# Kernel tuning notes

Hardware: AMD Instinct MI355X
Metric: run time of the kernel (lower is better)

## Reference

```python
import jax, jax.numpy as jnp
import numpy as np

B, S, D = 4, 2048, 1024
H = 16
HD = D // H          # 64
HALF = HD // 2       # 32


def _rope(t, cos, sin):
    # t: [B, S, H, HD]; cos/sin: [S, HALF]
    tr = t.reshape(*t.shape[:-1], HALF, 2)
    t0, t1 = tr[..., 0], tr[..., 1]
    c = cos[None, :, None, :]
    s = sin[None, :, None, :]
    out = jnp.stack([t0 * c - t1 * s, t0 * s + t1 * c], axis=-1)
    return out.reshape(t.shape)


def setup_inputs() -> dict:
    key = jax.random.key(0)
    ks = jax.random.split(key, 7)
    x = jax.random.normal(ks[0], (B, S, D), dtype=jnp.float32)
    # rotary tables (theta=10000 convention)
    inv_freq = 1.0 / (10000.0 ** (np.arange(0, HD, 2, dtype=np.float32) / HD))
    angles = np.arange(S, dtype=np.float32)[:, None] * inv_freq[None, :]
    freqs_cos = jnp.asarray(np.cos(angles))
    freqs_sin = jnp.asarray(np.sin(angles))
    scale = 1.0 / np.sqrt(D)
    wq = jax.random.normal(ks[1], (D, D), dtype=jnp.float32) * scale
    wk = jax.random.normal(ks[2], (D, D), dtype=jnp.float32) * scale
    wv = jax.random.normal(ks[3], (D, D), dtype=jnp.float32) * scale
    wo = jax.random.normal(ks[4], (D, D), dtype=jnp.float32) * scale
    return {"x": x, "freqs_cos": freqs_cos, "freqs_sin": freqs_sin,
            "wq": wq, "wk": wk, "wv": wv, "wo": wo}


def reference(x, freqs_cos, freqs_sin, wq, wk, wv, wo):
    b, s, d = x.shape
    q = (x @ wq.T).reshape(b, s, H, HD)
    k = (x @ wk.T).reshape(b, s, H, HD)
    v = (x @ wv.T).reshape(b, s, H, HD)
    q = _rope(q, freqs_cos, freqs_sin)
    k = _rope(k, freqs_cos, freqs_sin)
    # [B, H, S, HD]
    q = q.transpose(0, 2, 1, 3)
    k = k.transpose(0, 2, 1, 3)
    v = v.transpose(0, 2, 1, 3)
    scores = jnp.einsum("bhqd,bhkd->bhqk", q, k) / jnp.sqrt(jnp.float32(HD))
    causal = jnp.tril(jnp.ones((s, s), dtype=bool))
    scores = jnp.where(causal[None, None, :, :], scores, jnp.finfo(scores.dtype).min)
    attn = jax.nn.softmax(scores, axis=-1)
    out = jnp.einsum("bhqk,bhkd->bhqd", attn, v)
    out = out.transpose(0, 2, 1, 3).reshape(b, s, d)
    return out @ wo.T
```

## Files before the change

kernel.cpp:

```cpp
#include <hip/hip_runtime.h>
#include <hip/hip_bf16.h>
#include <cstdint>
#include <cstddef>

#define BB 4
#define SS 2048
#define DD 1024
#define HH 16
#define HDD 64

typedef __bf16 bf16_t;
typedef __bf16 bf16x8 __attribute__((ext_vector_type(8)));
typedef float f32x4 __attribute__((ext_vector_type(4)));
typedef unsigned u32x2 __attribute__((ext_vector_type(2)));

__device__ __forceinline__ unsigned short f2bf(float f) {
    unsigned u = __float_as_uint(f);
    unsigned r = (u + 0x7FFFu + ((u >> 16) & 1u)) >> 16;
    return (unsigned short)r;
}
__device__ __forceinline__ bf16_t f2bf16(float f) {
    return __builtin_bit_cast(bf16_t, f2bf(f));
}
__device__ __forceinline__ bf16x8 cvt8(float4 a, float4 b) {
    bf16x8 r;
    r[0] = f2bf16(a.x); r[1] = f2bf16(a.y);
    r[2] = f2bf16(a.z); r[3] = f2bf16(a.w);
    r[4] = f2bf16(b.x); r[5] = f2bf16(b.y);
    r[6] = f2bf16(b.z); r[7] = f2bf16(b.w);
    return r;
}
__device__ __forceinline__ unsigned cvtpk_bf16(float lo, float hi) {
    unsigned r;
    asm("v_cvt_pk_bf16_f32 %0, %1, %2" : "=v"(r) : "v"(lo), "v"(hi));
    return r;
}
__device__ __forceinline__ float exp2_raw(float x) {
    float r;
    asm("v_exp_f32 %0, %1" : "=v"(r) : "v"(x));
    return r;
}

#define GLL16(gp, lp)                                                          \
    __builtin_amdgcn_global_load_lds(                                          \
        (const __attribute__((address_space(1))) void*)(gp),                   \
        (__attribute__((address_space(3))) void*)(lp), 16, 0, 0)

__global__ __launch_bounds__(256) void cvt1(const float* __restrict__ in,
                                            bf16_t* __restrict__ out) {
    size_t i = (size_t)blockIdx.x * 256 + threadIdx.x;
    const float4* p = (const float4*)in + i * 2;
    *(bf16x8*)(out + i * 8) = cvt8(p[0], p[1]);
}
__global__ __launch_bounds__(256) void cvt4(
    const float* __restrict__ w0, const float* __restrict__ w1,
    const float* __restrict__ w2, const float* __restrict__ w3,
    bf16_t* __restrict__ o0, bf16_t* __restrict__ o1,
    bf16_t* __restrict__ o2, bf16_t* __restrict__ o3) {
    const float* in = blockIdx.y == 0 ? w0 : blockIdx.y == 1 ? w1
                    : blockIdx.y == 2 ? w2 : w3;
    bf16_t* out = blockIdx.y == 0 ? o0 : blockIdx.y == 1 ? o1
                : blockIdx.y == 2 ? o2 : o3;
    size_t i = (size_t)blockIdx.x * 256 + threadIdx.x;
    const float4* p = (const float4*)in + i * 2;
    *(bf16x8*)(out + i * 8) = cvt8(p[0], p[1]);
}

__global__ __launch_bounds__(256, 2) void gemm_qkv(
    const bf16_t* __restrict__ A, const bf16_t* __restrict__ Wall,
    bf16_t* __restrict__ Qb, bf16_t* __restrict__ Kb,
    bf16_t* __restrict__ Vt,
    const float* __restrict__ fcos, const float* __restrict__ fsin,
    float qscale)
{
    constexpr int K = 1024;
    __shared__ alignas(16) bf16_t lA[128 * 64];
    __shared__ alignas(16) bf16_t lB[128 * 64];

    const int tid  = threadIdx.x;
    const int w    = tid >> 6;
    const int lane = tid & 63;
    const int quad = lane >> 4;
    const int l16  = lane & 15;
    const int wm   = w >> 1;
    const int wn   = w & 1;
    const int m0   = blockIdx.y * 128;
    const int n0   = blockIdx.x * 128;
    const int sub  = n0 >> 10;

    f32x4 acc[4][4];
#pragma unroll
    for (int i = 0; i < 4; i++)
#pragma unroll
        for (int j = 0; j < 4; j++) acc[i][j] = (f32x4){0.f, 0.f, 0.f, 0.f};

    const int srow8 = lane >> 3;
    const int slot  = lane & 7;

    for (int k0 = 0; k0 < K; k0 += 64) {
#pragma unroll
        for (int i = 0; i < 4; ++i) {
            int row = w * 32 + i * 8;
            GLL16(A + (size_t)(m0 + row + srow8) * K + k0 + slot * 8,
                  &lA[row * 64]);
            GLL16(Wall + (size_t)(n0 + row + srow8) * K + k0 + slot * 8,
                  &lB[row * 64]);
        }
        __syncthreads();
#pragma unroll
        for (int kk = 0; kk < 2; ++kk) {
            bf16x8 af[4], bfr[4];
#pragma unroll
            for (int mt = 0; mt < 4; ++mt)
                af[mt] = *(const bf16x8*)
                    &lA[(wm * 64 + mt * 16 + l16) * 64 + (kk * 4 + quad) * 8];
#pragma unroll
            for (int nt = 0; nt < 4; ++nt)
                bfr[nt] = *(const bf16x8*)
                    &lB[(wn * 64 + nt * 16 + l16) * 64 + (kk * 4 + quad) * 8];
#pragma unroll
            for (int mt = 0; mt < 4; ++mt)
#pragma unroll
                for (int nt = 0; nt < 4; ++nt)
                    acc[mt][nt] = __builtin_amdgcn_mfma_f32_16x16x32_bf16(
                        af[mt], bfr[nt], acc[mt][nt], 0, 0, 0);
        }
        __syncthreads();
    }

    if (sub < 2) {
        unsigned short* Cu = (unsigned short*)(sub == 0 ? Qb : Kb);
        const float scale = sub == 0 ? qscale : 1.0f;
#pragma unroll
        for (int mt = 0; mt < 4; ++mt) {
#pragma unroll
            for (int nt = 0; nt < 4; ++nt) {
                int col  = (n0 & 1023) + wn * 64 + nt * 16 + l16;
                int h    = col >> 6;
                int d    = col & 63;
                int pidx = d >> 1;
                bool even = (col & 1) == 0;
#pragma unroll
                for (int r = 0; r < 4; ++r) {
                    int m = m0 + wm * 64 + mt * 16 + quad * 4 + r;
                    int b = m >> 11;
                    int s = m & 2047;
                    float v  = acc[mt][nt][r];
                    float p  = __shfl_xor(v, 1);
                    float c  = fcos[s * 32 + pidx];
                    float sn = fsin[s * 32 + pidx];
                    float o  = even ? (v * c - p * sn) : (p * sn + v * c);
                    Cu[(size_t)((b * HH + h) * SS + s) * HDD + d] =
                        f2bf(o * scale);
                }
            }
        }
    } else {
        unsigned short* Cu = (unsigned short*)Vt;
#pragma unroll
        for (int mt = 0; mt < 4; ++mt) {
#pragma unroll
            for (int nt = 0; nt < 4; ++nt) {
                int col = (n0 & 1023) + wn * 64 + nt * 16 + l16;
                int h = col >> 6, d = col & 63;
#pragma unroll
                for (int r = 0; r < 4; ++r) {
                    int m = m0 + wm * 64 + mt * 16 + quad * 4 + r;
                    int b = m >> 11, s = m & 2047;
                    Cu[(size_t)((b * HH + h) * HDD + d) * SS + s] =
                        f2bf(acc[mt][nt][r]);
                }
            }
        }
    }
}

__global__ __launch_bounds__(256, 2) void gemm_out(
    const bf16_t* __restrict__ A, const bf16_t* __restrict__ W,
    float* __restrict__ Cf)
{
    constexpr int K = 1024, N = 1024;
    __shared__ alignas(16) bf16_t lA[128 * 64];
    __shared__ alignas(16) bf16_t lB[128 * 64];

    const int tid  = threadIdx.x;
    const int w    = tid >> 6;
    const int lane = tid & 63;
    const int quad = lane >> 4;
    const int l16  = lane & 15;
    const int wm   = w >> 1;
    const int wn   = w & 1;
    const int m0   = blockIdx.y * 128;
    const int n0   = blockIdx.x * 128;

    f32x4 acc[4][4];
#pragma unroll
    for (int i = 0; i < 4; i++)
#pragma unroll
        for (int j = 0; j < 4; j++) acc[i][j] = (f32x4){0.f, 0.f, 0.f, 0.f};

    const int srow8 = lane >> 3;
    const int slot  = lane & 7;

    for (int k0 = 0; k0 < K; k0 += 64) {
#pragma unroll
        for (int i = 0; i < 4; ++i) {
            int row = w * 32 + i * 8;
            GLL16(A + (size_t)(m0 + row + srow8) * K + k0 + slot * 8,
                  &lA[row * 64]);
            GLL16(W + (size_t)(n0 + row + srow8) * K + k0 + slot * 8,
                  &lB[row * 64]);
        }
        __syncthreads();
#pragma unroll
        for (int kk = 0; kk < 2; ++kk) {
            bf16x8 af[4], bfr[4];
#pragma unroll
            for (int mt = 0; mt < 4; ++mt)
                af[mt] = *(const bf16x8*)
                    &lA[(wm * 64 + mt * 16 + l16) * 64 + (kk * 4 + quad) * 8];
#pragma unroll
            for (int nt = 0; nt < 4; ++nt)
                bfr[nt] = *(const bf16x8*)
                    &lB[(wn * 64 + nt * 16 + l16) * 64 + (kk * 4 + quad) * 8];
#pragma unroll
            for (int mt = 0; mt < 4; ++mt)
#pragma unroll
                for (int nt = 0; nt < 4; ++nt)
                    acc[mt][nt] = __builtin_amdgcn_mfma_f32_16x16x32_bf16(
                        af[mt], bfr[nt], acc[mt][nt], 0, 0, 0);
        }
        __syncthreads();
    }

#pragma unroll
    for (int mt = 0; mt < 4; ++mt) {
        int mrow = m0 + wm * 64 + mt * 16 + quad * 4;
#pragma unroll
        for (int nt = 0; nt < 4; ++nt) {
            int col = n0 + wn * 64 + nt * 16 + l16;
#pragma unroll
            for (int r = 0; r < 4; ++r)
                Cf[(size_t)(mrow + r) * N + col] = acc[mt][nt][r];
        }
    }
}

__global__ __launch_bounds__(256, 2) void attn(
    const bf16_t* __restrict__ Q, const bf16_t* __restrict__ Kt,
    const bf16_t* __restrict__ Vt, bf16_t* __restrict__ O)
{
    __shared__ alignas(16) bf16_t lK[128 * 64];
    __shared__ alignas(16) bf16_t lV[2][64 * 64];

    const int tid  = threadIdx.x;
    const int w    = tid >> 6;
    const int lane = tid & 63;
    const int quad = lane >> 4;
    const int l16  = lane & 15;

    const int blk  = blockIdx.x;
    const int xcd  = blk & 7;
    const int rest = blk >> 3;
    const int g    = rest & 7;
    const int bh   = ((rest >> 3) << 3) | xcd;

    const int b = bh >> 4, h = bh & 15;
    unsigned short* Ou = (unsigned short*)O;
    const bf16_t* Qb = Q  + (size_t)bh * SS * HDD;
    const bf16_t* Kb = Kt + (size_t)bh * SS * HDD;
    const bf16_t* Vb = Vt + (size_t)bh * HDD * SS;

    const int row8 = lane >> 3;
    const int chk  = lane & 7;

    for (int phase = 0; phase < 2; ++phase) {
        const int Tp  = phase ? 15 - g : g;
        const int q0  = Tp * 128 + w * 32;
        const int nkb = Tp + 1;

        bf16x8 qf[2][2];
#pragma unroll
        for (int qs = 0; qs < 2; ++qs) {
            const bf16_t* qp =
                Qb + (size_t)(q0 + qs * 16 + l16) * HDD + quad * 8;
            qf[qs][0] = *(const bf16x8*)(qp);
            qf[qs][1] = *(const bf16x8*)(qp + 32);
        }

        f32x4 o[2][4];
        float ps[2];
#pragma unroll
        for (int qs = 0; qs < 2; ++qs) {
            ps[qs] = 0.f;
#pragma unroll
            for (int i = 0; i < 4; ++i) o[qs][i] = (f32x4){0.f, 0.f, 0.f, 0.f};
        }

        for (int t = 0; t < nkb; ++t) {
            const int kb2 = t * 128;

#pragma unroll
            for (int i = 0; i < 4; ++i) {
                int rbase = w * 32 + i * 8;
                int row   = rbase + row8;
                GLL16(Kb + (size_t)(kb2 + row) * HDD + ((chk ^ (row & 7)) * 8),
                      &lK[rbase * 64]);
            }
#pragma unroll
            for (int pp = 0; pp < 2; ++pp)
#pragma unroll
                for (int i = 0; i < 2; ++i) {
                    int rbase = w * 16 + i * 8;
                    int row   = rbase + row8;
                    GLL16(Vb + (size_t)row * SS + kb2 + pp * 64 +
                              ((chk ^ (row & 7)) * 8),
                          &lV[pp][rbase * 64]);
                }
            __syncthreads();

#pragma unroll
            for (int p = 0; p < 2; ++p) {
                const int kbp = kb2 + p * 64;
                if (kbp < q0 + 32) {
                    const bool diag = (kbp + 63 > q0);

                    bf16x8 kf[4][2];
#pragma unroll
                    for (int nt = 0; nt < 4; ++nt) {
                        const int row = p * 64 + nt * 16 + l16;
#pragma unroll
                        for (int hf = 0; hf < 2; ++hf)
                            kf[nt][hf] = *(const bf16x8*)
                                &lK[row * 64 +
                                    (((hf * 4 + quad) ^ (row & 7)) * 8)];
                    }

                    unsigned pk[4][2][2];
#pragma unroll
                    for (int nt = 0; nt < 4; ++nt) {
                        const int krow = kbp + nt * 16 + quad * 4;
#pragma unroll
                        for (int qs = 0; qs < 2; ++qs) {
                            f32x4 s = (f32x4){0.f, 0.f, 0.f, 0.f};
                            s = __builtin_amdgcn_mfma_f32_16x16x32_bf16(
                                kf[nt][0], qf[qs][0], s, 0, 0, 0);
                            s = __builtin_amdgcn_mfma_f32_16x16x32_bf16(
                                kf[nt][1], qf[qs][1], s, 0, 0, 0);
                            if (diag) {
                                const int qcol = q0 + qs * 16 + l16;
#pragma unroll
                                for (int r = 0; r < 4; ++r)
                                    if (krow + r > qcol) s[r] = -1e30f;
                            }
                            float ev[4];
#pragma unroll
                            for (int r = 0; r < 4; ++r) {
                                float e = exp2_raw(s[r]);
                                ps[qs] += e;
                                ev[r] = e;
                            }
                            pk[nt][qs][0] = cvtpk_bf16(ev[0], ev[1]);
                            pk[nt][qs][1] = cvtpk_bf16(ev[2], ev[3]);
                        }
                    }

#pragma unroll
                    for (int kk = 0; kk < 2; ++kk) {
                        bf16x8 vfk[4];
#pragma unroll
                        for (int nt = 0; nt < 4; ++nt) {
                            const int row = nt * 16 + l16;
                            vfk[nt] = *(const bf16x8*)
                                &lV[p][row * 64 +
                                       (((kk * 4 + quad) ^ (row & 7)) * 8)];
                        }
#pragma unroll
                        for (int qs = 0; qs < 2; ++qs) {
                            u32x2 sA = __builtin_amdgcn_permlane32_swap(
                                pk[2 * kk][qs][0], pk[2 * kk + 1][qs][0],
                                false, false);
                            u32x2 sB = __builtin_amdgcn_permlane32_swap(
                                pk[2 * kk][qs][1], pk[2 * kk + 1][qs][1],
                                false, false);
                            u32x2 tA = __builtin_amdgcn_permlane16_swap(
                                sA.x, sA.y, false, false);
                            u32x2 tB = __builtin_amdgcn_permlane16_swap(
                                sB.x, sB.y, false, false);
                            union { unsigned d[4]; bf16x8 v; } pf;
                            pf.d[0] = tA.x;
                            pf.d[1] = tB.x;
                            pf.d[2] = tA.y;
                            pf.d[3] = tB.y;
#pragma unroll
                            for (int nt = 0; nt < 4; ++nt)
                                o[qs][nt] =
                                    __builtin_amdgcn_mfma_f32_16x16x32_bf16(
                                        pf.v, vfk[nt], o[qs][nt], 0, 0, 0);
                        }
                    }
                }
            }
            __syncthreads();
        }

#pragma unroll
        for (int qs = 0; qs < 2; ++qs) {
            float tsum = ps[qs];
            tsum += __shfl_xor(tsum, 16);
            tsum += __shfl_xor(tsum, 32);
            float inv[4];
#pragma unroll
            for (int r = 0; r < 4; ++r)
                inv[r] = 1.0f / __shfl(tsum, quad * 4 + r);
#pragma unroll
            for (int nt = 0; nt < 4; ++nt) {
                int d = nt * 16 + l16;
#pragma unroll
                for (int r = 0; r < 4; ++r) {
                    int s = q0 + qs * 16 + quad * 4 + r;
                    Ou[(size_t)(b * SS + s) * DD + h * HDD + d] =
                        f2bf(o[qs][nt][r] * inv[r]);
                }
            }
        }
    }
}

extern "C" void kernel_launch(void* const* d_in, const int* in_sizes, int n_in,
                              void* d_out, int out_size, void* d_ws,
                              size_t ws_size, hipStream_t stream)
{
    const float* x    = (const float*)d_in[0];
    const float* fcos = (const float*)d_in[1];
    const float* fsin = (const float*)d_in[2];
    const float* wq   = (const float*)d_in[3];
    const float* wk   = (const float*)d_in[4];
    const float* wv   = (const float*)d_in[5];
    const float* wo   = (const float*)d_in[6];

    char* ws = (char*)d_ws;
    const size_t TSZ = (size_t)BB * SS * DD * sizeof(bf16_t);
    const size_t WSZ = (size_t)DD * DD * sizeof(bf16_t);
    bf16_t* Qb  = (bf16_t*)(ws);
    bf16_t* Kb  = (bf16_t*)(ws + TSZ);
    bf16_t* Ob  = (bf16_t*)(ws + 2 * TSZ);
    bf16_t* wb0 = (bf16_t*)(ws + 3 * TSZ);
    bf16_t* wb1 = (bf16_t*)(ws + 3 * TSZ + WSZ);
    bf16_t* wb2 = (bf16_t*)(ws + 3 * TSZ + 2 * WSZ);
    bf16_t* wb3 = (bf16_t*)(ws + 3 * TSZ + 3 * WSZ);
    bf16_t* xb  = (bf16_t*)d_out;
    bf16_t* Vt  = (bf16_t*)((char*)d_out + TSZ);

    dim3 bb(256);
    cvt1<<<dim3(4096), bb, 0, stream>>>(x, xb);
    cvt4<<<dim3(512, 4), bb, 0, stream>>>(wq, wk, wv, wo, wb0, wb1, wb2, wb3);

    const float sscale = 0.125f * 1.44269504088896f;
    gemm_qkv<<<dim3(24, 64), bb, 0, stream>>>(xb, wb0, Qb, Kb, Vt,
                                              fcos, fsin, sscale);
    attn<<<dim3(512), bb, 0, stream>>>(Qb, Kb, Vt, Ob);
    gemm_out<<<dim3(8, 64), bb, 0, stream>>>(Ob, wb3, (float*)d_out);
}
```

Measured before the change: 251.0 us.

## XOR-swizzle GEMM LDS tiles, remap block order per XCD, merge conversion kernels

Applies an XOR swizzle to the 16-byte chunk index when staging A and B tiles into LDS and when reading them back, so MFMA fragment reads spread across banks instead of conflicting. Remaps the linear block index in both GEMMs so consecutive blocks dispatched to the same XCD cover nearby tiles, which should improve L2 reuse. Merges the input and weight fp32-to-bf16 conversion kernels into one launch. The remap assumes round-robin dispatch across eight XCDs and grid sizes divisible by eight.

```diff
diff --git a/kernel.cpp b/kernel.cpp
--- a/kernel.cpp
+++ b/kernel.cpp
@@ -46,22 +46,28 @@
         (const __attribute__((address_space(1))) void*)(gp),                   \
         (__attribute__((address_space(3))) void*)(lp), 16, 0, 0)
 
-__global__ __launch_bounds__(256) void cvt1(const float* __restrict__ in,
-                                            bf16_t* __restrict__ out) {
-    size_t i = (size_t)blockIdx.x * 256 + threadIdx.x;
-    const float4* p = (const float4*)in + i * 2;
-    *(bf16x8*)(out + i * 8) = cvt8(p[0], p[1]);
-}
-__global__ __launch_bounds__(256) void cvt4(
+__global__ __launch_bounds__(256) void cvtall(
+    const float* __restrict__ x,
     const float* __restrict__ w0, const float* __restrict__ w1,
     const float* __restrict__ w2, const float* __restrict__ w3,
+    bf16_t* __restrict__ xb,
     bf16_t* __restrict__ o0, bf16_t* __restrict__ o1,
-    bf16_t* __restrict__ o2, bf16_t* __restrict__ o3) {
-    const float* in = blockIdx.y == 0 ? w0 : blockIdx.y == 1 ? w1
-                    : blockIdx.y == 2 ? w2 : w3;
-    bf16_t* out = blockIdx.y == 0 ? o0 : blockIdx.y == 1 ? o1
-                : blockIdx.y == 2 ? o2 : o3;
-    size_t i = (size_t)blockIdx.x * 256 + threadIdx.x;
+    bf16_t* __restrict__ o2, bf16_t* __restrict__ o3)
+{
+    const int bx = blockIdx.x;
+    const float* in;
+    bf16_t* out;
+    size_t i;
+    if (bx < 4096) {
+        in = x; out = xb;
+        i = (size_t)bx * 256 + threadIdx.x;
+    } else {
+        const int g = bx - 4096;
+        const int s = g >> 9;
+        in  = s == 0 ? w0 : s == 1 ? w1 : s == 2 ? w2 : w3;
+        out = s == 0 ? o0 : s == 1 ? o1 : s == 2 ? o2 : o3;
+        i = (size_t)(g & 511) * 256 + threadIdx.x;
+    }
     const float4* p = (const float4*)in + i * 2;
     *(bf16x8*)(out + i * 8) = cvt8(p[0], p[1]);
 }
@@ -84,9 +90,12 @@
     const int l16  = lane & 15;
     const int wm   = w >> 1;
     const int wn   = w & 1;
-    const int m0   = blockIdx.y * 128;
-    const int n0   = blockIdx.x * 128;
-    const int sub  = n0 >> 10;
+
+    const int lid     = blockIdx.y * 24 + blockIdx.x;
+    const int logical = (lid & 7) * 192 + (lid >> 3);
+    const int m0      = (logical / 24) * 128;
+    const int n0      = (logical % 24) * 128;
+    const int sub     = n0 >> 10;
 
     f32x4 acc[4][4];
 #pragma unroll
@@ -100,24 +109,28 @@
     for (int k0 = 0; k0 < K; k0 += 64) {
 #pragma unroll
         for (int i = 0; i < 4; ++i) {
-            int row = w * 32 + i * 8;
-            GLL16(A + (size_t)(m0 + row + srow8) * K + k0 + slot * 8,
-                  &lA[row * 64]);
-            GLL16(Wall + (size_t)(n0 + row + srow8) * K + k0 + slot * 8,
-                  &lB[row * 64]);
+            int rbase = w * 32 + i * 8;
+            int row   = rbase + srow8;
+            int sc    = (slot ^ (row & 7)) * 8;
+            GLL16(A + (size_t)(m0 + row) * K + k0 + sc, &lA[rbase * 64]);
+            GLL16(Wall + (size_t)(n0 + row) * K + k0 + sc, &lB[rbase * 64]);
         }
         __syncthreads();
 #pragma unroll
         for (int kk = 0; kk < 2; ++kk) {
             bf16x8 af[4], bfr[4];
 #pragma unroll
-            for (int mt = 0; mt < 4; ++mt)
+            for (int mt = 0; mt < 4; ++mt) {
+                const int row = wm * 64 + mt * 16 + l16;
                 af[mt] = *(const bf16x8*)
-                    &lA[(wm * 64 + mt * 16 + l16) * 64 + (kk * 4 + quad) * 8];
-#pragma unroll
-            for (int nt = 0; nt < 4; ++nt)
+                    &lA[row * 64 + (((kk * 4 + quad) ^ (row & 7)) * 8)];
+            }
+#pragma unroll
+            for (int nt = 0; nt < 4; ++nt) {
+                const int row = wn * 64 + nt * 16 + l16;
                 bfr[nt] = *(const bf16x8*)
-                    &lB[(wn * 64 + nt * 16 + l16) * 64 + (kk * 4 + quad) * 8];
+                    &lB[row * 64 + (((kk * 4 + quad) ^ (row & 7)) * 8)];
+            }
 #pragma unroll
             for (int mt = 0; mt < 4; ++mt)
 #pragma unroll
@@ -190,8 +203,11 @@
     const int l16  = lane & 15;
     const int wm   = w >> 1;
     const int wn   = w & 1;
-    const int m0   = blockIdx.y * 128;
-    const int n0   = blockIdx.x * 128;
+
+    const int lid     = blockIdx.y * 8 + blockIdx.x;
+    const int logical = (lid & 7) * 64 + (lid >> 3);
+    const int m0      = (logical >> 3) * 128;
+    const int n0      = (logical & 7) * 128;
 
     f32x4 acc[4][4];
 #pragma unroll
@@ -205,24 +221,28 @@
     for (int k0 = 0; k0 < K; k0 += 64) {
 #pragma unroll
         for (int i = 0; i < 4; ++i) {
-            int row = w * 32 + i * 8;
-            GLL16(A + (size_t)(m0 + row + srow8) * K + k0 + slot * 8,
-                  &lA[row * 64]);
-            GLL16(W + (size_t)(n0 + row + srow8) * K + k0 + slot * 8,
-                  &lB[row * 64]);
+            int rbase = w * 32 + i * 8;
+            int row   = rbase + srow8;
+            int sc    = (slot ^ (row & 7)) * 8;
+            GLL16(A + (size_t)(m0 + row) * K + k0 + sc, &lA[rbase * 64]);
+            GLL16(W + (size_t)(n0 + row) * K + k0 + sc, &lB[rbase * 64]);
         }
         __syncthreads();
 #pragma unroll
         for (int kk = 0; kk < 2; ++kk) {
             bf16x8 af[4], bfr[4];
 #pragma unroll
-            for (int mt = 0; mt < 4; ++mt)
+            for (int mt = 0; mt < 4; ++mt) {
+                const int row = wm * 64 + mt * 16 + l16;
                 af[mt] = *(const bf16x8*)
-                    &lA[(wm * 64 + mt * 16 + l16) * 64 + (kk * 4 + quad) * 8];
-#pragma unroll
-            for (int nt = 0; nt < 4; ++nt)
+                    &lA[row * 64 + (((kk * 4 + quad) ^ (row & 7)) * 8)];
+            }
+#pragma unroll
+            for (int nt = 0; nt < 4; ++nt) {
+                const int row = wn * 64 + nt * 16 + l16;
                 bfr[nt] = *(const bf16x8*)
-                    &lB[(wn * 64 + nt * 16 + l16) * 64 + (kk * 4 + quad) * 8];
+                    &lB[row * 64 + (((kk * 4 + quad) ^ (row & 7)) * 8)];
+            }
 #pragma unroll
             for (int mt = 0; mt < 4; ++mt)
 #pragma unroll
@@ -453,8 +473,8 @@
     bf16_t* Vt  = (bf16_t*)((char*)d_out + TSZ);
 
     dim3 bb(256);
-    cvt1<<<dim3(4096), bb, 0, stream>>>(x, xb);
-    cvt4<<<dim3(512, 4), bb, 0, stream>>>(wq, wk, wv, wo, wb0, wb1, wb2, wb3);
+    cvtall<<<dim3(6144), bb, 0, stream>>>(x, wq, wk, wv, wo,
+                                          xb, wb0, wb1, wb2, wb3);
 
     const float sscale = 0.125f * 1.44269504088896f;
     gemm_qkv<<<dim3(24, 64), bb, 0, stream>>>(xb, wb0, Qb, Kb, Vt,
```

Result: faster. 229.6 us (-8.5%).
